# Kernel optimization log

Measured on AMD Instinct MI355X. Metric: run time of the kernel, lower is better.

Reference implementation:

```python
import jax, jax.numpy as jnp
import numpy as np

CH, KS, PAD = 64, 3, 1
B, H, W = 4, 128, 128
EH, EW = 64, 64
K = KS * KS


def setup_inputs() -> dict:
    key = jax.random.key(0)
    ks = jax.random.split(key, 10)
    C = CH
    z = lambda *s: jnp.zeros(s, jnp.float32)
    return {
        "ev_feat": jax.random.normal(ks[0], (B, C, EH, EW), jnp.float32),
        "im_feat": jax.random.normal(ks[1], (B, C, H, W), jnp.float32),
        "mlp_w0": jax.random.normal(ks[2], (2 * C + 4, C), jnp.float32) * 0.05,
        "mlp_b0": z(C),
        "mlp_w1": jax.random.normal(ks[3], (C, C), jnp.float32) * 0.05,
        "mlp_b1": z(C),
        "mlp_w2": jax.random.normal(ks[4], (C, C), jnp.float32) * 0.05,
        "mlp_b2": z(C),
        "mlp_w3": jax.random.normal(ks[5], (C, C), jnp.float32) * 0.05,
        "mlp_b3": z(C),
        "off_w": jax.random.normal(ks[6], (3 * K, C, KS, KS), jnp.float32) * 0.01,
        "off_b": z(3 * K),
        "dcn_w": jax.random.normal(ks[7], (C, C, KS, KS), jnp.float32) * 0.05,
        "dcn_b": z(C),
    }


def _conv(x, w, b):
    y = jax.lax.conv_general_dilated(x, w, (1, 1), [(PAD, PAD), (PAD, PAD)],
                                     dimension_numbers=("NCHW", "OIHW", "NCHW"))
    return y + b[None, :, None, None]


def _forward(ev_feat, im_feat, mlp_w0, mlp_b0, mlp_w1, mlp_b1, mlp_w2, mlp_b2,
             mlp_w3, mlp_b3, off_w, off_b, dcn_w, dcn_b):
    C = CH
    Bn = im_feat.shape[0]
    Q = H * W
    # ---- coordinate-conditioned MLP: LIIF-style nearest query of ev_feat ----
    ys = -1.0 + (2.0 * jnp.arange(H, dtype=jnp.float32) + 1.0) / H  # pixel centers in [-1,1]
    xs = -1.0 + (2.0 * jnp.arange(W, dtype=jnp.float32) + 1.0) / W
    gy, gx = jnp.meshgrid(ys, xs, indexing="ij")
    coord = jnp.stack([gy, gx], -1).reshape(-1, 2)  # (Q,2) as (y,x), torch make_coord order
    iy = jnp.clip(jnp.round(((coord[:, 0] + 1.0) * EH - 1.0) / 2.0), 0, EH - 1).astype(jnp.int32)
    ix = jnp.clip(jnp.round(((coord[:, 1] + 1.0) * EW - 1.0) / 2.0), 0, EW - 1).astype(jnp.int32)
    q_feat = ev_feat[:, :, iy, ix].transpose(0, 2, 1)  # (B,Q,C) nearest-sampled event feature
    q_coord = jnp.stack([-1.0 + (2.0 * iy + 1.0) / EH, -1.0 + (2.0 * ix + 1.0) / EW], -1)
    rel = (coord - q_coord) * jnp.array([EH, EW], jnp.float32)  # (Q,2) rel coord scaled by feat res
    rel_cell = jnp.array([2.0 / H * EH, 2.0 / W * EW], jnp.float32)  # cell * feat res
    q_im = im_feat.reshape(Bn, C, Q).transpose(0, 2, 1)  # (B,Q,C); coords are im_feat pixel centers
    inp = jnp.concatenate([q_feat, q_im,
                           jnp.broadcast_to(rel, (Bn, Q, 2)),
                           jnp.broadcast_to(rel_cell, (Bn, Q, 2))], -1)  # (B,Q,2C+4)
    x = jax.nn.relu(inp @ mlp_w0 + mlp_b0)
    x = jax.nn.relu(x @ mlp_w1 + mlp_b1)
    x = jax.nn.relu(x @ mlp_w2 + mlp_b2)
    x = x @ mlp_w3 + mlp_b3  # (B,Q,C)
    feat = x.reshape(Bn, H, W, C).transpose(0, 3, 1, 2)  # (B,C,H,W)
    # ---- ModulatedDeformConvPack (DCNv2) ----
    oo = _conv(feat, off_w, off_b)  # (B,3K,H,W)
    o1, o2, m = oo[:, :K], oo[:, K:2 * K], oo[:, 2 * K:]
    off = jnp.concatenate([o1, o2], 1)  # (B,2K,H,W), interleaved (y,x) per kernel tap
    off_y, off_x = off[:, 0::2], off[:, 1::2]  # (B,K,H,W)
    mask = jax.nn.sigmoid(m)  # (B,K,H,W)
    ky = (jnp.arange(K) // KS - PAD).astype(jnp.float32)
    kx = (jnp.arange(K) % KS - PAD).astype(jnp.float32)
    py = jnp.arange(H, dtype=jnp.float32)[None, :, None] + ky[:, None, None] + off_y  # (B,K,H,W)
    px = jnp.arange(W, dtype=jnp.float32)[None, None, :] + kx[:, None, None] + off_x
    y0 = jnp.floor(py)
    x0 = jnp.floor(px)
    ly = py - y0
    lx = px - x0

    def gather(yi, xi):
        valid = (yi >= 0) & (yi <= H - 1) & (xi >= 0) & (xi <= W - 1)
        yc = jnp.clip(yi, 0, H - 1).astype(jnp.int32)
        xc = jnp.clip(xi, 0, W - 1).astype(jnp.int32)
        v = jax.vmap(lambda img, yy, xx: img[:, yy, xx])(feat, yc, xc)  # (B,C,K,H,W)
        return v * valid[:, None].astype(feat.dtype)

    w00 = ((1 - ly) * (1 - lx))[:, None]
    w01 = ((1 - ly) * lx)[:, None]
    w10 = (ly * (1 - lx))[:, None]
    w11 = (ly * lx)[:, None]
    samp = (gather(y0, x0) * w00 + gather(y0, x0 + 1) * w01 +
            gather(y0 + 1, x0) * w10 + gather(y0 + 1, x0 + 1) * w11)  # (B,C,K,H,W)
    samp = samp * mask[:, None]
    out = jnp.einsum("bckhw,ock->bohw", samp, dcn_w.reshape(C, C, K))
    return out + dcn_b[None, :, None, None]


def reference(ev_feat, im_feat, mlp_w0, mlp_b0, mlp_w1, mlp_b1, mlp_w2, mlp_b2,
              mlp_w3, mlp_b3, off_w, off_b, dcn_w, dcn_b):
    return _forward(ev_feat, im_feat, mlp_w0, mlp_b0, mlp_w1, mlp_b1, mlp_w2, mlp_b2,
                    mlp_w3, mlp_b3, off_w, off_b, dcn_w, dcn_b)
```

## Files before the change

### kernel.cpp

```cpp
#include <hip/hip_runtime.h>
#include <math.h>

#define CCH 64
#define HH  128
#define WW  128
#define NB  4
#define NPIX (NB*HH*WW)
#define NWG  (NPIX/64)

__device__ __forceinline__ int swz_block(int bid) {
    return (bid & 7) * (NWG >> 3) + (bid >> 3);
}

__global__ __launch_bounds__(256) void prep_kernel(
    const float* __restrict__ off_w, const float* __restrict__ dcn_w,
    float* __restrict__ offT, float* __restrict__ dcnT)
{
    int idx = blockIdx.x * 256 + threadIdx.x;
    if (idx < 576 * 28) {
        int rc = idx / 28;
        int o  = idx % 28;
        offT[rc * 28 + o] = (o < 27) ? off_w[o * 576 + rc] : 0.0f;
    }
    if (idx < 36864) {
        int o    = idx & 63;
        int rest = idx >> 6;
        int ic   = rest & 63;
        int k    = rest >> 6;
        dcnT[(k * 64 + ic) * 64 + o] = dcn_w[o * 576 + ic * 9 + k];
    }
}

__global__ __launch_bounds__(256) void mlp_kernel(
    const float* __restrict__ ev, const float* __restrict__ im,
    const float* __restrict__ w0, const float* __restrict__ b0,
    const float* __restrict__ w1, const float* __restrict__ b1,
    const float* __restrict__ w2, const float* __restrict__ b2,
    const float* __restrict__ w3, const float* __restrict__ b3,
    float* __restrict__ feat)
{
    __shared__ float xA[64 * 64];
    __shared__ float xB[64 * 64];
    int tid  = threadIdx.x;
    int cg   = __builtin_amdgcn_readfirstlane(tid >> 6);
    int lane = tid & 63;
    int p = swz_block(blockIdx.x) * 64 + lane;
    int b = p >> 14;
    int q = p & 16383;
    int h = q >> 7;
    int w = q & 127;
    int c0 = cg * 16;

    float acc[16];
#pragma unroll
    for (int j = 0; j < 16; ++j) acc[j] = b0[c0 + j];

    const float* evb = ev + ((b * 64) * 64 + (h >> 1)) * 64 + (w >> 1);
    for (int i = 0; i < 64; ++i) {
        float v = evb[i * 4096];
        const float* wr = w0 + i * 64 + c0;
#pragma unroll
        for (int j = 0; j < 16; ++j) acc[j] = fmaf(v, wr[j], acc[j]);
    }
    const float* imb = im + ((b * 64) * 128 + h) * 128 + w;
    for (int i = 0; i < 64; ++i) {
        float v = imb[i * 16384];
        const float* wr = w0 + (64 + i) * 64 + c0;
#pragma unroll
        for (int j = 0; j < 16; ++j) acc[j] = fmaf(v, wr[j], acc[j]);
    }
    {
        float rely = (h & 1) ? 0.5f : -0.5f;
        float relx = (w & 1) ? 0.5f : -0.5f;
        const float* wr = w0 + 128 * 64 + c0;
#pragma unroll
        for (int j = 0; j < 16; ++j) acc[j] = fmaf(rely, wr[j], acc[j]);
#pragma unroll
        for (int j = 0; j < 16; ++j) acc[j] = fmaf(relx, wr[64 + j], acc[j]);
#pragma unroll
        for (int j = 0; j < 16; ++j) acc[j] += wr[128 + j] + wr[192 + j];
    }
#pragma unroll
    for (int j = 0; j < 16; ++j) xA[(c0 + j) * 64 + lane] = fmaxf(acc[j], 0.0f);
    __syncthreads();

#pragma unroll
    for (int j = 0; j < 16; ++j) acc[j] = b1[c0 + j];
    for (int i = 0; i < 64; ++i) {
        float v = xA[i * 64 + lane];
        const float* wr = w1 + i * 64 + c0;
#pragma unroll
        for (int j = 0; j < 16; ++j) acc[j] = fmaf(v, wr[j], acc[j]);
    }
#pragma unroll
    for (int j = 0; j < 16; ++j) xB[(c0 + j) * 64 + lane] = fmaxf(acc[j], 0.0f);
    __syncthreads();

#pragma unroll
    for (int j = 0; j < 16; ++j) acc[j] = b2[c0 + j];
    for (int i = 0; i < 64; ++i) {
        float v = xB[i * 64 + lane];
        const float* wr = w2 + i * 64 + c0;
#pragma unroll
        for (int j = 0; j < 16; ++j) acc[j] = fmaf(v, wr[j], acc[j]);
    }
#pragma unroll
    for (int j = 0; j < 16; ++j) xA[(c0 + j) * 64 + lane] = fmaxf(acc[j], 0.0f);
    __syncthreads();

#pragma unroll
    for (int j = 0; j < 16; ++j) acc[j] = b3[c0 + j];
    for (int i = 0; i < 64; ++i) {
        float v = xA[i * 64 + lane];
        const float* wr = w3 + i * 64 + c0;
#pragma unroll
        for (int j = 0; j < 16; ++j) acc[j] = fmaf(v, wr[j], acc[j]);
    }
    float* fb = feat + (b * 64 + c0) * 16384 + q;
#pragma unroll
    for (int j = 0; j < 16; ++j) fb[j * 16384] = acc[j];
}

__global__ __launch_bounds__(256) void off_kernel(
    const float* __restrict__ feat, const float* __restrict__ offT,
    const float* __restrict__ off_b,
    float* __restrict__ oo)
{
    __shared__ float po[4 * 27 * 64];
    int tid  = threadIdx.x;
    int wv   = __builtin_amdgcn_readfirstlane(tid >> 6);
    int lane = tid & 63;
    int p = swz_block(blockIdx.x) * 64 + lane;
    int b = p >> 14;
    int q = p & 16383;
    int h = q >> 7;
    int w = q & 127;
    int c0 = wv * 16;

    float acc[27];
#pragma unroll
    for (int o = 0; o < 27; ++o) acc[o] = 0.0f;

    const float* fb = feat + (b * 64 + c0) * 16384;
    for (int i = 0; i < 16; ++i) {
        const float* f = fb + i * 16384;
        float v[9];
#pragma unroll
        for (int ky = 0; ky < 3; ++ky)
#pragma unroll
            for (int kx = 0; kx < 3; ++kx) {
                int y = h + ky - 1, x = w + kx - 1;
                bool ok = (y >= 0) && (y < 128) && (x >= 0) && (x < 128);
                v[ky * 3 + kx] = ok ? f[y * 128 + x] : 0.0f;
            }
#pragma unroll
        for (int kk = 0; kk < 9; ++kk) {
            const float* wr = offT + ((c0 + i) * 9 + kk) * 28;
#pragma unroll
            for (int o = 0; o < 27; ++o) acc[o] = fmaf(v[kk], wr[o], acc[o]);
        }
    }

#pragma unroll
    for (int o = 0; o < 27; ++o) po[(wv * 27 + o) * 64 + lane] = acc[o];
    __syncthreads();

#pragma unroll
    for (int j = 0; j < 7; ++j) {
        int o = wv + 4 * j;
        if (o < 27) {
            float s = off_b[o]
                    + po[o * 64 + lane] + po[(27 + o) * 64 + lane]
                    + po[(54 + o) * 64 + lane] + po[(81 + o) * 64 + lane];
            oo[((b * 27 + o) << 14) + q] = s;
        }
    }
}

__global__ __launch_bounds__(256) void dcn_kernel(
    const float* __restrict__ feat,
    const float* __restrict__ oo,
    const float* __restrict__ dcnT, const float* __restrict__ dcn_b,
    float* __restrict__ out)
{
    __shared__ float sbuf[64 * 64];
    int tid  = threadIdx.x;
    int wv   = __builtin_amdgcn_readfirstlane(tid >> 6);
    int lane = tid & 63;
    int p = swz_block(blockIdx.x) * 64 + lane;
    int b = p >> 14;
    int q = p & 16383;
    int h = q >> 7;
    int w = q & 127;
    int c0 = wv * 16;

    float acc[16];
#pragma unroll
    for (int j = 0; j < 16; ++j) acc[j] = dcn_b[c0 + j];

    const float* fb  = feat + (b * 64 + c0) * 16384;
    const float* oob = oo + ((b * 27) << 14) + q;

    for (int k = 0; k < 9; ++k) {
        float oy = oob[(2 * k) << 14];
        float ox = oob[(2 * k + 1) << 14];
        float ml = 1.0f / (1.0f + expf(-oob[(18 + k) << 14]));
        float py = (float)(h + k / 3 - 1) + oy;
        float px = (float)(w + k % 3 - 1) + ox;

        float y0f = floorf(py), x0f = floorf(px);
        float ly = py - y0f, lx = px - x0f;
        int y0 = (int)y0f, x0 = (int)x0f;

        bool vy0 = (y0f >= 0.0f)        && (y0f <= 127.0f);
        bool vy1 = (y0f + 1.0f >= 0.0f) && (y0f + 1.0f <= 127.0f);
        bool vx0 = (x0f >= 0.0f)        && (x0f <= 127.0f);
        bool vx1 = (x0f + 1.0f >= 0.0f) && (x0f + 1.0f <= 127.0f);

        int yc0 = min(max(y0, 0), 127),     yc1 = min(max(y0 + 1, 0), 127);
        int xc0 = min(max(x0, 0), 127),     xc1 = min(max(x0 + 1, 0), 127);

        float w00 = (1.0f - ly) * (1.0f - lx) * ml * ((vy0 && vx0) ? 1.0f : 0.0f);
        float w01 = (1.0f - ly) * lx          * ml * ((vy0 && vx1) ? 1.0f : 0.0f);
        float w10 = ly * (1.0f - lx)          * ml * ((vy1 && vx0) ? 1.0f : 0.0f);
        float w11 = ly * lx                   * ml * ((vy1 && vx1) ? 1.0f : 0.0f);

        int i00 = yc0 * 128 + xc0, i01 = yc0 * 128 + xc1;
        int i10 = yc1 * 128 + xc0, i11 = yc1 * 128 + xc1;

#pragma unroll 8
        for (int i = 0; i < 16; ++i) {
            const float* f = fb + i * 16384;
            float s = w00 * f[i00] + w01 * f[i01] + w10 * f[i10] + w11 * f[i11];
            sbuf[(c0 + i) * 64 + lane] = s;
        }
        __syncthreads();

        const float* wk = dcnT + (k * 64) * 64 + c0;
#pragma unroll 4
        for (int ic = 0; ic < 64; ++ic) {
            float s = sbuf[ic * 64 + lane];
            const float* wr = wk + ic * 64;
#pragma unroll
            for (int j = 0; j < 16; ++j) acc[j] = fmaf(s, wr[j], acc[j]);
        }
        __syncthreads();
    }

    float* ob = out + (b * 64 + c0) * 16384 + q;
#pragma unroll
    for (int j = 0; j < 16; ++j) ob[j * 16384] = acc[j];
}

extern "C" void kernel_launch(void* const* d_in, const int* in_sizes, int n_in,
                              void* d_out, int out_size, void* d_ws, size_t ws_size,
                              hipStream_t stream)
{
    const float* ev    = (const float*)d_in[0];
    const float* im    = (const float*)d_in[1];
    const float* w0    = (const float*)d_in[2];
    const float* b0    = (const float*)d_in[3];
    const float* w1    = (const float*)d_in[4];
    const float* b1    = (const float*)d_in[5];
    const float* w2    = (const float*)d_in[6];
    const float* b2    = (const float*)d_in[7];
    const float* w3    = (const float*)d_in[8];
    const float* b3    = (const float*)d_in[9];
    const float* off_w = (const float*)d_in[10];
    const float* off_b = (const float*)d_in[11];
    const float* dcn_w = (const float*)d_in[12];
    const float* dcn_b = (const float*)d_in[13];
    float* out = (float*)d_out;

    char* ws = (char*)d_ws;
    float* feat  = (float*)(ws);
    float* oo    = (float*)(ws + 16777216);
    float* offT  = (float*)(ws + 23855104);
    float* dcnT  = (float*)(ws + 23920640);

    prep_kernel<<<144, 256, 0, stream>>>(off_w, dcn_w, offT, dcnT);
    mlp_kernel<<<NWG, 256, 0, stream>>>(ev, im, w0, b0, w1, b1, w2, b2,
                                        w3, b3, feat);
    off_kernel<<<NWG, 256, 0, stream>>>(feat, offT, off_b, oo);
    dcn_kernel<<<NWG, 256, 0, stream>>>(feat, oo, dcnT, dcn_b, out);
}
```

Measured before the change: 186.0 us.

## Double-buffer DCN sampling to overlap next-tap gathers with current-tap FMA

Splits the LDS sample buffer into two halves (sA/sB) and software-pipelines the 9-tap loop. The bilinear gathers for tap k+1 are issued in two halves of 8 channels, interleaved with the two halves of the 64-channel FMA reduction for tap k. This halves the barriers per tap and hides global gather latency behind arithmetic. In exchange it doubles LDS use and adds 32 prefetch registers per thread, which may reduce occupancy.

```diff
diff --git a/kernel.cpp b/kernel.cpp
--- a/kernel.cpp
+++ b/kernel.cpp
@@ -177,13 +177,46 @@
     }
 }
 
+__device__ __forceinline__ void dcn_transform(
+    const float* oob, int k, int h, int w,
+    float& W00, float& W01, float& W10, float& W11,
+    int& i00, int& i01, int& i10, int& i11)
+{
+    float oy = oob[(2 * k) << 14];
+    float ox = oob[(2 * k + 1) << 14];
+    float ml = 1.0f / (1.0f + expf(-oob[(18 + k) << 14]));
+    float py = (float)(h + k / 3 - 1) + oy;
+    float px = (float)(w + k % 3 - 1) + ox;
+
+    float y0f = floorf(py), x0f = floorf(px);
+    float ly = py - y0f, lx = px - x0f;
+    int y0 = (int)y0f, x0 = (int)x0f;
+
+    bool vy0 = (y0f >= 0.0f)        && (y0f <= 127.0f);
+    bool vy1 = (y0f + 1.0f >= 0.0f) && (y0f + 1.0f <= 127.0f);
+    bool vx0 = (x0f >= 0.0f)        && (x0f <= 127.0f);
+    bool vx1 = (x0f + 1.0f >= 0.0f) && (x0f + 1.0f <= 127.0f);
+
+    int yc0 = min(max(y0, 0), 127),     yc1 = min(max(y0 + 1, 0), 127);
+    int xc0 = min(max(x0, 0), 127),     xc1 = min(max(x0 + 1, 0), 127);
+
+    W00 = (1.0f - ly) * (1.0f - lx) * ml * ((vy0 && vx0) ? 1.0f : 0.0f);
+    W01 = (1.0f - ly) * lx          * ml * ((vy0 && vx1) ? 1.0f : 0.0f);
+    W10 = ly * (1.0f - lx)          * ml * ((vy1 && vx0) ? 1.0f : 0.0f);
+    W11 = ly * lx                   * ml * ((vy1 && vx1) ? 1.0f : 0.0f);
+
+    i00 = yc0 * 128 + xc0; i01 = yc0 * 128 + xc1;
+    i10 = yc1 * 128 + xc0; i11 = yc1 * 128 + xc1;
+}
+
 __global__ __launch_bounds__(256) void dcn_kernel(
     const float* __restrict__ feat,
     const float* __restrict__ oo,
     const float* __restrict__ dcnT, const float* __restrict__ dcn_b,
     float* __restrict__ out)
 {
-    __shared__ float sbuf[64 * 64];
+    __shared__ float sA[64 * 64];
+    __shared__ float sB[64 * 64];
     int tid  = threadIdx.x;
     int wv   = __builtin_amdgcn_readfirstlane(tid >> 6);
     int lane = tid & 63;
@@ -201,50 +234,73 @@
     const float* fb  = feat + (b * 64 + c0) * 16384;
     const float* oob = oo + ((b * 27) << 14) + q;
 
-    for (int k = 0; k < 9; ++k) {
-        float oy = oob[(2 * k) << 14];
-        float ox = oob[(2 * k + 1) << 14];
-        float ml = 1.0f / (1.0f + expf(-oob[(18 + k) << 14]));
-        float py = (float)(h + k / 3 - 1) + oy;
-        float px = (float)(w + k % 3 - 1) + ox;
-
-        float y0f = floorf(py), x0f = floorf(px);
-        float ly = py - y0f, lx = px - x0f;
-        int y0 = (int)y0f, x0 = (int)x0f;
-
-        bool vy0 = (y0f >= 0.0f)        && (y0f <= 127.0f);
-        bool vy1 = (y0f + 1.0f >= 0.0f) && (y0f + 1.0f <= 127.0f);
-        bool vx0 = (x0f >= 0.0f)        && (x0f <= 127.0f);
-        bool vx1 = (x0f + 1.0f >= 0.0f) && (x0f + 1.0f <= 127.0f);
-
-        int yc0 = min(max(y0, 0), 127),     yc1 = min(max(y0 + 1, 0), 127);
-        int xc0 = min(max(x0, 0), 127),     xc1 = min(max(x0 + 1, 0), 127);
-
-        float w00 = (1.0f - ly) * (1.0f - lx) * ml * ((vy0 && vx0) ? 1.0f : 0.0f);
-        float w01 = (1.0f - ly) * lx          * ml * ((vy0 && vx1) ? 1.0f : 0.0f);
-        float w10 = ly * (1.0f - lx)          * ml * ((vy1 && vx0) ? 1.0f : 0.0f);
-        float w11 = ly * lx                   * ml * ((vy1 && vx1) ? 1.0f : 0.0f);
-
-        int i00 = yc0 * 128 + xc0, i01 = yc0 * 128 + xc1;
-        int i10 = yc1 * 128 + xc0, i11 = yc1 * 128 + xc1;
-
+    {
+        float W00, W01, W10, W11; int i00, i01, i10, i11;
+        dcn_transform(oob, 0, h, w, W00, W01, W10, W11, i00, i01, i10, i11);
 #pragma unroll 8
         for (int i = 0; i < 16; ++i) {
             const float* f = fb + i * 16384;
-            float s = w00 * f[i00] + w01 * f[i01] + w10 * f[i10] + w11 * f[i11];
-            sbuf[(c0 + i) * 64 + lane] = s;
-        }
+            float s = W00 * f[i00] + W01 * f[i01] + W10 * f[i10] + W11 * f[i11];
+            sA[(c0 + i) * 64 + lane] = s;
+        }
+    }
+    __syncthreads();
+
+    float* cur = sA;
+    float* nxt = sB;
+
+    for (int k = 0; k < 9; ++k) {
+        bool pre = (k < 8);
+        float W00, W01, W10, W11; int i00, i01, i10, i11;
+        float r00[8], r01[8], r10[8], r11[8];
+
+        if (pre) {
+            dcn_transform(oob, k + 1, h, w, W00, W01, W10, W11, i00, i01, i10, i11);
+#pragma unroll
+            for (int i = 0; i < 8; ++i) {
+                const float* f = fb + i * 16384;
+                r00[i] = f[i00]; r01[i] = f[i01]; r10[i] = f[i10]; r11[i] = f[i11];
+            }
+        }
+
+        const float* wk = dcnT + (k * 64) * 64 + c0;
+#pragma unroll 8
+        for (int ic = 0; ic < 32; ++ic) {
+            float s = cur[ic * 64 + lane];
+            const float* wr = wk + ic * 64;
+#pragma unroll
+            for (int j = 0; j < 16; ++j) acc[j] = fmaf(s, wr[j], acc[j]);
+        }
+
+        if (pre) {
+#pragma unroll
+            for (int i = 0; i < 8; ++i)
+                nxt[(c0 + i) * 64 + lane] =
+                    W00 * r00[i] + W01 * r01[i] + W10 * r10[i] + W11 * r11[i];
+#pragma unroll
+            for (int i = 0; i < 8; ++i) {
+                const float* f = fb + (8 + i) * 16384;
+                r00[i] = f[i00]; r01[i] = f[i01]; r10[i] = f[i10]; r11[i] = f[i11];
+            }
+        }
+
+#pragma unroll 8
+        for (int ic = 32; ic < 64; ++ic) {
+            float s = cur[ic * 64 + lane];
+            const float* wr = wk + ic * 64;
+#pragma unroll
+            for (int j = 0; j < 16; ++j) acc[j] = fmaf(s, wr[j], acc[j]);
+        }
+
+        if (pre) {
+#pragma unroll
+            for (int i = 0; i < 8; ++i)
+                nxt[(c0 + 8 + i) * 64 + lane] =
+                    W00 * r00[i] + W01 * r01[i] + W10 * r10[i] + W11 * r11[i];
+        }
+
         __syncthreads();
-
-        const float* wk = dcnT + (k * 64) * 64 + c0;
-#pragma unroll 4
-        for (int ic = 0; ic < 64; ++ic) {
-            float s = sbuf[ic * 64 + lane];
-            const float* wr = wk + ic * 64;
-#pragma unroll
-            for (int j = 0; j < 16; ++j) acc[j] = fmaf(s, wr[j], acc[j]);
-        }
-        __syncthreads();
+        float* t = cur; cur = nxt; nxt = t;
     }
 
     float* ob = out + (b * 64 + c0) * 16384 + q;
```

New measurement: 182.1 us. -2.1%, faster.
